# Performance work log

Measured on AMD Instinct MI355X. Metric: run time of the kernel, lower is better.

## Reference

```python
import jax, jax.numpy as jnp
import numpy as np

B, S, D_IN, D_OUT = 4, 2048, 1024, 1024


def setup_inputs() -> dict:
    key = jax.random.key(0)
    ks = jax.random.split(key, 7)
    s_in = 1.0 / np.sqrt(D_IN)
    return {
        "x": jax.random.normal(ks[0], (B, S, D_IN), dtype=jnp.float32),
        "Wq": jax.random.uniform(ks[1], (D_IN, D_OUT), jnp.float32, -s_in, s_in),
        "bq": jax.random.uniform(ks[2], (D_OUT,), jnp.float32, -s_in, s_in),
        "Wk": jax.random.uniform(ks[3], (D_IN, D_OUT), jnp.float32, -s_in, s_in),
        "bk": jax.random.uniform(ks[4], (D_OUT,), jnp.float32, -s_in, s_in),
        "Wv": jax.random.uniform(ks[5], (D_IN, D_OUT), jnp.float32, -s_in, s_in),
        "bv": jax.random.uniform(ks[6], (D_OUT,), jnp.float32, -s_in, s_in),
    }


def reference(x, Wq, bq, Wk, bk, Wv, bv):
    # Linear projections (torch Linear: x @ W^T + b; here W stored as [in,out])
    q = x @ Wq + bq  # [B,S,D]
    k = x @ Wk + bk
    v = x @ Wv + bv
    scores = jnp.einsum("bqd,bkd->bqk", q, k)  # [B,S,S]
    # causal mask: positions j > i masked with -inf (applied BEFORE scaling,
    # which is equivalent since -inf/sqrt(d) == -inf)
    seq = scores.shape[-1]
    causal = jnp.tril(jnp.ones((seq, seq), dtype=bool))
    masked = jnp.where(causal, scores, -jnp.inf)
    attn = jax.nn.softmax(masked / np.sqrt(k.shape[-1]), axis=-1)
    # dropout p=0.0 -> identity
    return attn @ v  # [B,S,D]
```

## Files before the change

kernel.cpp:

```cpp
#include <hip/hip_runtime.h>

typedef unsigned short u16;
typedef unsigned int u32;
typedef __attribute__((ext_vector_type(8))) short short8;
typedef __attribute__((ext_vector_type(4))) float f32x4;

__device__ __forceinline__ u16 f2bf(float f) {
    u32 u = __float_as_uint(f);
    u32 r = (u + 0x7fffu + ((u >> 16) & 1u)) >> 16;
    return (u16)r;
}
__device__ __forceinline__ float bf2f(u16 h) {
    return __uint_as_float(((u32)h) << 16);
}

__device__ __forceinline__ void gld16(u16* lds_dst, const u16* g_src) {
    __builtin_amdgcn_global_load_lds(
        (const __attribute__((address_space(1))) unsigned int*)g_src,
        (__attribute__((address_space(3))) unsigned int*)lds_dst,
        16, 0, 0);
}

__global__ void split_x_k(const float* __restrict__ x, u16* __restrict__ xh,
                          u16* __restrict__ xl) {
    long i = ((long)blockIdx.x * 256 + threadIdx.x) * 4;
    float4 f = *(const float4*)(x + i);
    u16 h0 = f2bf(f.x), h1 = f2bf(f.y), h2 = f2bf(f.z), h3 = f2bf(f.w);
    u16 l0 = f2bf(f.x - bf2f(h0)), l1 = f2bf(f.y - bf2f(h1));
    u16 l2 = f2bf(f.z - bf2f(h2)), l3 = f2bf(f.w - bf2f(h3));
    uint2 hv, lv;
    hv.x = (u32)h0 | ((u32)h1 << 16); hv.y = (u32)h2 | ((u32)h3 << 16);
    lv.x = (u32)l0 | ((u32)l1 << 16); lv.y = (u32)l2 | ((u32)l3 << 16);
    *(uint2*)(xh + i) = hv;
    *(uint2*)(xl + i) = lv;
}

__global__ void splitT_w_k(const float* __restrict__ Wq, const float* __restrict__ Wk,
                           const float* __restrict__ Wv, u16* __restrict__ wth,
                           u16* __restrict__ wtl) {
    __shared__ float tile[32][33];
    int z = blockIdx.z;
    const float* W = (z == 0) ? Wq : (z == 1) ? Wk : Wv;
    int n0 = blockIdx.x * 32, k0 = blockIdx.y * 32;
    int tx = threadIdx.x, ty = threadIdx.y;
#pragma unroll
    for (int r0 = 0; r0 < 4; ++r0) {
        int r = ty + r0 * 8;
        tile[r][tx] = W[(long)(k0 + r) * 1024 + n0 + tx];
    }
    __syncthreads();
    long zoff = (long)z * 1024 * 1024;
#pragma unroll
    for (int r0 = 0; r0 < 4; ++r0) {
        int r = ty + r0 * 8;
        float f = tile[tx][r];
        u16 h = f2bf(f), l = f2bf(f - bf2f(h));
        long idx = zoff + (long)(n0 + r) * 1024 + k0 + tx;
        wth[idx] = h;
        wtl[idx] = l;
    }
}

__global__ void transpose_v_k(const u16* __restrict__ vh, const u16* __restrict__ vl,
                              u16* __restrict__ vth, u16* __restrict__ vtl) {
    __shared__ u16 th[32][33];
    __shared__ u16 tl[32][33];
    int z = blockIdx.z;
    int d0 = blockIdx.x * 32, s0 = blockIdx.y * 32;
    int tx = threadIdx.x, ty = threadIdx.y;
#pragma unroll
    for (int r0 = 0; r0 < 4; ++r0) {
        int r = ty + r0 * 8;
        long idx = ((long)z * 2048 + s0 + r) * 1024 + d0 + tx;
        th[r][tx] = vh[idx];
        tl[r][tx] = vl[idx];
    }
    __syncthreads();
    long zoff = (long)z * 1024 * 2048;
#pragma unroll
    for (int r0 = 0; r0 < 4; ++r0) {
        int r = ty + r0 * 8;
        long idx = zoff + (long)(d0 + r) * 2048 + s0 + tx;
        vth[idx] = th[tx][r];
        vtl[idx] = tl[tx][r];
    }
}

template <int MODE, int NF>
__launch_bounds__(512, 2)
__global__ void gemm_k(const u16* __restrict__ Ah, const u16* __restrict__ Al, long sAz,
                       const u16* __restrict__ Bh, const u16* __restrict__ Bl, long sBz,
                       int lda, int ldb, int Ksize,
                       float* __restrict__ outF, long sCz, int ldc,
                       u16* __restrict__ oh0, u16* __restrict__ oh1, u16* __restrict__ oh2,
                       u16* __restrict__ ol0, u16* __restrict__ ol1, u16* __restrict__ ol2,
                       const float* __restrict__ b0, const float* __restrict__ b1,
                       const float* __restrict__ b2) {
    constexpr int BN = NF * 64;
    constexpr int SLOT = 8192 + NF * 4096;
    constexpr int RING = (MODE == 0) ? 3 : 2;
    __shared__ u16 lds[RING * SLOT];

    const int bi = (MODE == 2) ? (gridDim.x - 1 - (int)blockIdx.x) : blockIdx.x;
    const int bj = blockIdx.y, z = blockIdx.z;
    if (MODE == 1 && bj > bi) return;
    int nsteps = Ksize / 32;
    if (MODE == 2) nsteps = min(nsteps, (bi + 1) * 4);

    const u16* gA_h = Ah + (long)z * sAz;
    const u16* gA_l = Al + (long)z * sAz;
    const u16* gB_h = Bh + (long)z * sBz;
    const u16* gB_l = Bl + (long)z * sBz;

    const int tid = threadIdx.x;
    const int lane = tid & 63, w = tid >> 6;
    const int wr = w >> 2, wc = w & 3;

    const int srow = tid >> 2;
    const int ls8 = (((tid & 3) ^ ((tid >> 3) & 3)) << 3);
    const long aoff  = ((long)bi * 128 + srow) * lda + ls8;
    const long boff0 = ((long)bj * BN + srow) * ldb + ls8;
    const long boff1 = boff0 + 128L * (long)ldb;
    const int wbase = w * 512;

    f32x4 acc[4][NF] = {};

    const int fr = lane & 15;
    const int ps8 = (((lane >> 4) ^ ((fr >> 1) & 3)) << 3);

    auto stage = [&](int slot, int step) {
        const int k0 = step * 32;
        u16* sb = lds + slot * SLOT;
        gld16(sb + wbase,              gA_h + aoff + k0);
        gld16(sb + 4096 + wbase,       gA_l + aoff + k0);
        gld16(sb + 8192 + wbase,       gB_h + boff0 + k0);
        if constexpr (NF == 4) gld16(sb + 12288 + wbase, gB_h + boff1 + k0);
        gld16(sb + 8192 + NF * 2048 + wbase, gB_l + boff0 + k0);
        if constexpr (NF == 4) gld16(sb + 8192 + NF * 2048 + 4096 + wbase, gB_l + boff1 + k0);
    };

    auto compute = [&](int slot) {
        const u16* LA = lds + slot * SLOT;
        const u16* LB = LA + 8192;
        short8 afh[4], afl[4], bfh[NF], bfl[NF];
#pragma unroll
        for (int m = 0; m < 4; ++m) {
            int off = (wr * 64 + m * 16 + fr) * 32 + ps8;
            afh[m] = *(const short8*)(LA + off);
            afl[m] = *(const short8*)(LA + 4096 + off);
        }
#pragma unroll
        for (int n = 0; n < NF; ++n) {
            int off = (wc * (NF * 16) + n * 16 + fr) * 32 + ps8;
            bfh[n] = *(const short8*)(LB + off);
            bfl[n] = *(const short8*)(LB + NF * 2048 + off);
        }
        __builtin_amdgcn_s_setprio(1);
#pragma unroll
        for (int m = 0; m < 4; ++m)
#pragma unroll
            for (int n = 0; n < NF; ++n) {
                acc[m][n] = __builtin_amdgcn_mfma_f32_16x16x32_bf16(afh[m], bfh[n], acc[m][n], 0, 0, 0);
                acc[m][n] = __builtin_amdgcn_mfma_f32_16x16x32_bf16(afh[m], bfl[n], acc[m][n], 0, 0, 0);
                acc[m][n] = __builtin_amdgcn_mfma_f32_16x16x32_bf16(afl[m], bfh[n], acc[m][n], 0, 0, 0);
            }
        __builtin_amdgcn_s_setprio(0);
    };

    if constexpr (MODE == 0) {
        stage(0, 0);
        if (nsteps > 1) stage(1, 1);
        int cs = 0, ns = 2;
        for (int h = 0; h < nsteps; ++h) {
            if (h + 1 < nsteps) {
                asm volatile("s_waitcnt vmcnt(6)" ::: "memory");
            } else {
                asm volatile("s_waitcnt vmcnt(0)" ::: "memory");
            }
            __builtin_amdgcn_s_barrier();
            __builtin_amdgcn_sched_barrier(0);
            if (h + 2 < nsteps) stage(ns, h + 2);
            compute(cs);
            cs = (cs == 2) ? 0 : cs + 1;
            ns = (ns == 2) ? 0 : ns + 1;
        }
    } else {
        stage(0, 0);
        int cs = 0;
        for (int h = 0; h < nsteps; ++h) {
            asm volatile("s_waitcnt vmcnt(0)" ::: "memory");
            __builtin_amdgcn_s_barrier();
            __builtin_amdgcn_sched_barrier(0);
            if (h + 1 < nsteps) stage(cs ^ 1, h + 1);
            compute(cs);
            cs ^= 1;
        }
    }

    const int row0 = bi * 128 + wr * 64 + (lane >> 4) * 4;
    const int col0 = bj * BN + wc * (NF * 16) + (lane & 15);

    if (MODE == 0) {
        const float* bias = (z == 0) ? b0 : (z == 1) ? b1 : b2;
        u16* oh = (z == 0) ? oh0 : (z == 1) ? oh1 : oh2;
        u16* ol = (z == 0) ? ol0 : (z == 1) ? ol1 : ol2;
#pragma unroll
        for (int n = 0; n < NF; ++n) {
            float bv = bias[col0 + n * 16];
#pragma unroll
            for (int m = 0; m < 4; ++m)
#pragma unroll
                for (int j = 0; j < 4; ++j) {
                    float v = acc[m][n][j] + bv;
                    long idx = (long)(row0 + m * 16 + j) * ldc + col0 + n * 16;
                    u16 h = f2bf(v);
                    oh[idx] = h;
                    ol[idx] = f2bf(v - bf2f(h));
                }
        }
    } else {
        float* o = outF + (long)z * sCz;
#pragma unroll
        for (int m = 0; m < 4; ++m)
#pragma unroll
            for (int n = 0; n < NF; ++n)
#pragma unroll
                for (int j = 0; j < 4; ++j)
                    o[(long)(row0 + m * 16 + j) * ldc + col0 + n * 16] = acc[m][n][j];
    }
}

__global__ void softmax_k(const float* __restrict__ S, u16* __restrict__ Ph,
                          u16* __restrict__ Pl) {
    const long row = blockIdx.x;
    const int i = (int)(row & 2047);
    const float* srow = S + row * 2048;
    u16* ph = Ph + row * 2048;
    u16* pl = Pl + row * 2048;
    const int t = threadIdx.x;
    const int limit = ((i >> 7) + 1) << 7;

    float v[8];
    float m = -1e30f;
#pragma unroll
    for (int j = 0; j < 8; ++j) {
        int c = j * 256 + t;
        float x = (c <= i) ? srow[c] : -1e30f;
        v[j] = x;
        m = fmaxf(m, x);
    }
#pragma unroll
    for (int off = 32; off; off >>= 1) m = fmaxf(m, __shfl_xor(m, off));
    __shared__ float redm[4], reds[4];
    if ((t & 63) == 0) redm[t >> 6] = m;
    __syncthreads();
    m = fmaxf(fmaxf(redm[0], redm[1]), fmaxf(redm[2], redm[3]));

    float p[8];
    float s = 0.f;
#pragma unroll
    for (int j = 0; j < 8; ++j) {
        int c = j * 256 + t;
        float e = (c <= i) ? __expf((v[j] - m) * 0.03125f) : 0.f;
        p[j] = e;
        s += e;
    }
#pragma unroll
    for (int off = 32; off; off >>= 1) s += __shfl_xor(s, off);
    if ((t & 63) == 0) reds[t >> 6] = s;
    __syncthreads();
    s = reds[0] + reds[1] + reds[2] + reds[3];
    const float inv = 1.f / s;
#pragma unroll
    for (int j = 0; j < 8; ++j) {
        int c = j * 256 + t;
        if (c < limit) {
            float o = p[j] * inv;
            u16 h = f2bf(o);
            ph[c] = h;
            pl[c] = f2bf(o - bf2f(h));
        }
    }
}

extern "C" void kernel_launch(void* const* d_in, const int* in_sizes, int n_in,
                              void* d_out, int out_size, void* d_ws, size_t ws_size,
                              hipStream_t stream) {
    const float* x  = (const float*)d_in[0];
    const float* Wq = (const float*)d_in[1];
    const float* bq = (const float*)d_in[2];
    const float* Wk = (const float*)d_in[3];
    const float* bk = (const float*)d_in[4];
    const float* Wv = (const float*)d_in[5];
    const float* bv = (const float*)d_in[6];
    float* out = (float*)d_out;
    char* ws = (char*)d_ws;
    const size_t MB = 1ull << 20;

    u16* xs_hi = (u16*)(ws + 0 * MB);
    u16* xs_lo = (u16*)(ws + 16 * MB);
    u16* wt_hi = (u16*)(ws + 32 * MB);
    u16* wt_lo = (u16*)(ws + 38 * MB);
    float* S   = (float*)(ws + 0 * MB);
    u16* q_hi = (u16*)(ws + 64 * MB);
    u16* q_lo = (u16*)(ws + 80 * MB);
    u16* k_hi = (u16*)(ws + 96 * MB);
    u16* k_lo = (u16*)(ws + 112 * MB);
    u16* P_hi = (u16*)(ws + 64 * MB);
    u16* P_lo = (u16*)(ws + 96 * MB);
    u16* v_hi  = (u16*)(ws + 128 * MB);
    u16* v_lo  = (u16*)(ws + 144 * MB);
    u16* vt_hi = (u16*)(ws + 160 * MB);
    u16* vt_lo = (u16*)(ws + 176 * MB);

    split_x_k<<<8192, 256, 0, stream>>>(x, xs_hi, xs_lo);
    splitT_w_k<<<dim3(32, 32, 3), dim3(32, 8), 0, stream>>>(Wq, Wk, Wv, wt_hi, wt_lo);
    gemm_k<0, 4><<<dim3(64, 4, 3), 512, 0, stream>>>(
        xs_hi, xs_lo, 0L, wt_hi, wt_lo, 1024L * 1024, 1024, 1024, 1024,
        nullptr, 0L, 1024, q_hi, k_hi, v_hi, q_lo, k_lo, v_lo, bq, bk, bv);
    transpose_v_k<<<dim3(32, 64, 4), dim3(32, 8), 0, stream>>>(v_hi, v_lo, vt_hi, vt_lo);
    gemm_k<1, 2><<<dim3(16, 16, 4), 512, 0, stream>>>(
        q_hi, q_lo, 2048L * 1024, k_hi, k_lo, 2048L * 1024, 1024, 1024, 1024,
        S, 2048L * 2048, 2048, nullptr, nullptr, nullptr, nullptr, nullptr, nullptr,
        nullptr, nullptr, nullptr);
    softmax_k<<<8192, 256, 0, stream>>>(S, P_hi, P_lo);
    gemm_k<2, 2><<<dim3(16, 8, 4), 512, 0, stream>>>(
        P_hi, P_lo, 2048L * 2048, vt_hi, vt_lo, 1024L * 2048, 2048, 2048, 2048,
        out, 2048L * 1024, 1024, nullptr, nullptr, nullptr, nullptr, nullptr, nullptr,
        nullptr, nullptr, nullptr);
}
```

Measured before the change: 443.9 us.

## Fuse softmax normalization into PV GEMM via row statistics kernel

Splits softmax into a row-reduction kernel that stores only the max and inverse sum per row, and moves the exponentiation and bf16 hi/lo split of P into the PV GEMM, which reads fp32 scores, converts them in registers and writes them straight to LDS. This removes writing and re-reading the two bf16 P matrices. The QK kernel also gains a block-index swizzle for locality. The templated GEMM is specialised into dedicated kernels. In exchange the PV kernel loads fp32 S (twice the bytes of bf16) and recomputes exp per tile. Its loop is serialized on a vmcnt(0) wait plus register writes to LDS, which may reduce overlap.

```diff
diff --git a/kernel.cpp b/kernel.cpp
--- a/kernel.cpp
+++ b/kernel.cpp
@@ -86,31 +86,25 @@
     }
 }
 
-template <int MODE, int NF>
 __launch_bounds__(512, 2)
-__global__ void gemm_k(const u16* __restrict__ Ah, const u16* __restrict__ Al, long sAz,
-                       const u16* __restrict__ Bh, const u16* __restrict__ Bl, long sBz,
-                       int lda, int ldb, int Ksize,
-                       float* __restrict__ outF, long sCz, int ldc,
+__global__ void gemm_k(const u16* __restrict__ Ah, const u16* __restrict__ Al,
+                       const u16* __restrict__ Bh, const u16* __restrict__ Bl,
                        u16* __restrict__ oh0, u16* __restrict__ oh1, u16* __restrict__ oh2,
                        u16* __restrict__ ol0, u16* __restrict__ ol1, u16* __restrict__ ol2,
                        const float* __restrict__ b0, const float* __restrict__ b1,
                        const float* __restrict__ b2) {
-    constexpr int BN = NF * 64;
+    constexpr int NF = 4;
+    constexpr int BN = 256;
     constexpr int SLOT = 8192 + NF * 4096;
-    constexpr int RING = (MODE == 0) ? 3 : 2;
-    __shared__ u16 lds[RING * SLOT];
-
-    const int bi = (MODE == 2) ? (gridDim.x - 1 - (int)blockIdx.x) : blockIdx.x;
-    const int bj = blockIdx.y, z = blockIdx.z;
-    if (MODE == 1 && bj > bi) return;
-    int nsteps = Ksize / 32;
-    if (MODE == 2) nsteps = min(nsteps, (bi + 1) * 4);
-
-    const u16* gA_h = Ah + (long)z * sAz;
-    const u16* gA_l = Al + (long)z * sAz;
-    const u16* gB_h = Bh + (long)z * sBz;
-    const u16* gB_l = Bl + (long)z * sBz;
+    __shared__ u16 lds[3 * SLOT];
+
+    const int bi = blockIdx.x, bj = blockIdx.y, z = blockIdx.z;
+    const int nsteps = 32;
+
+    const u16* gA_h = Ah;
+    const u16* gA_l = Al;
+    const u16* gB_h = Bh + (long)z * 1024 * 1024;
+    const u16* gB_l = Bl + (long)z * 1024 * 1024;
 
     const int tid = threadIdx.x;
     const int lane = tid & 63, w = tid >> 6;
@@ -118,9 +112,9 @@
 
     const int srow = tid >> 2;
     const int ls8 = (((tid & 3) ^ ((tid >> 3) & 3)) << 3);
-    const long aoff  = ((long)bi * 128 + srow) * lda + ls8;
-    const long boff0 = ((long)bj * BN + srow) * ldb + ls8;
-    const long boff1 = boff0 + 128L * (long)ldb;
+    const long aoff  = ((long)bi * 128 + srow) * 1024 + ls8;
+    const long boff0 = ((long)bj * BN + srow) * 1024 + ls8;
+    const long boff1 = boff0 + 128L * 1024;
     const int wbase = w * 512;
 
     f32x4 acc[4][NF] = {};
@@ -131,12 +125,12 @@
     auto stage = [&](int slot, int step) {
         const int k0 = step * 32;
         u16* sb = lds + slot * SLOT;
-        gld16(sb + wbase,              gA_h + aoff + k0);
-        gld16(sb + 4096 + wbase,       gA_l + aoff + k0);
-        gld16(sb + 8192 + wbase,       gB_h + boff0 + k0);
-        if constexpr (NF == 4) gld16(sb + 12288 + wbase, gB_h + boff1 + k0);
-        gld16(sb + 8192 + NF * 2048 + wbase, gB_l + boff0 + k0);
-        if constexpr (NF == 4) gld16(sb + 8192 + NF * 2048 + 4096 + wbase, gB_l + boff1 + k0);
+        gld16(sb + wbase,               gA_h + aoff + k0);
+        gld16(sb + 4096 + wbase,        gA_l + aoff + k0);
+        gld16(sb + 8192 + wbase,        gB_h + boff0 + k0);
+        gld16(sb + 12288 + wbase,       gB_h + boff1 + k0);
+        gld16(sb + 16384 + wbase,       gB_l + boff0 + k0);
+        gld16(sb + 20480 + wbase,       gB_l + boff1 + k0);
     };
 
     auto compute = [&](int slot) {
@@ -167,78 +161,142 @@
         __builtin_amdgcn_s_setprio(0);
     };
 
-    if constexpr (MODE == 0) {
-        stage(0, 0);
-        if (nsteps > 1) stage(1, 1);
-        int cs = 0, ns = 2;
-        for (int h = 0; h < nsteps; ++h) {
-            if (h + 1 < nsteps) {
-                asm volatile("s_waitcnt vmcnt(6)" ::: "memory");
-            } else {
-                asm volatile("s_waitcnt vmcnt(0)" ::: "memory");
-            }
-            __builtin_amdgcn_s_barrier();
-            __builtin_amdgcn_sched_barrier(0);
-            if (h + 2 < nsteps) stage(ns, h + 2);
-            compute(cs);
-            cs = (cs == 2) ? 0 : cs + 1;
-            ns = (ns == 2) ? 0 : ns + 1;
-        }
-    } else {
-        stage(0, 0);
-        int cs = 0;
-        for (int h = 0; h < nsteps; ++h) {
+    stage(0, 0);
+    stage(1, 1);
+    int cs = 0, ns = 2;
+    for (int h = 0; h < nsteps; ++h) {
+        if (h + 1 < nsteps) {
+            asm volatile("s_waitcnt vmcnt(6)" ::: "memory");
+        } else {
             asm volatile("s_waitcnt vmcnt(0)" ::: "memory");
-            __builtin_amdgcn_s_barrier();
-            __builtin_amdgcn_sched_barrier(0);
-            if (h + 1 < nsteps) stage(cs ^ 1, h + 1);
-            compute(cs);
-            cs ^= 1;
-        }
+        }
+        __builtin_amdgcn_s_barrier();
+        __builtin_amdgcn_sched_barrier(0);
+        if (h + 2 < nsteps) stage(ns, h + 2);
+        compute(cs);
+        cs = (cs == 2) ? 0 : cs + 1;
+        ns = (ns == 2) ? 0 : ns + 1;
     }
 
     const int row0 = bi * 128 + wr * 64 + (lane >> 4) * 4;
     const int col0 = bj * BN + wc * (NF * 16) + (lane & 15);
 
-    if (MODE == 0) {
-        const float* bias = (z == 0) ? b0 : (z == 1) ? b1 : b2;
-        u16* oh = (z == 0) ? oh0 : (z == 1) ? oh1 : oh2;
-        u16* ol = (z == 0) ? ol0 : (z == 1) ? ol1 : ol2;
-#pragma unroll
-        for (int n = 0; n < NF; ++n) {
-            float bv = bias[col0 + n * 16];
-#pragma unroll
-            for (int m = 0; m < 4; ++m)
-#pragma unroll
-                for (int j = 0; j < 4; ++j) {
-                    float v = acc[m][n][j] + bv;
-                    long idx = (long)(row0 + m * 16 + j) * ldc + col0 + n * 16;
-                    u16 h = f2bf(v);
-                    oh[idx] = h;
-                    ol[idx] = f2bf(v - bf2f(h));
-                }
-        }
-    } else {
-        float* o = outF + (long)z * sCz;
+    const float* bias = (z == 0) ? b0 : (z == 1) ? b1 : b2;
+    u16* oh = (z == 0) ? oh0 : (z == 1) ? oh1 : oh2;
+    u16* ol = (z == 0) ? ol0 : (z == 1) ? ol1 : ol2;
+#pragma unroll
+    for (int n = 0; n < NF; ++n) {
+        float bv = bias[col0 + n * 16];
 #pragma unroll
         for (int m = 0; m < 4; ++m)
 #pragma unroll
-            for (int n = 0; n < NF; ++n)
-#pragma unroll
-                for (int j = 0; j < 4; ++j)
-                    o[(long)(row0 + m * 16 + j) * ldc + col0 + n * 16] = acc[m][n][j];
-    }
-}
-
-__global__ void softmax_k(const float* __restrict__ S, u16* __restrict__ Ph,
-                          u16* __restrict__ Pl) {
+            for (int j = 0; j < 4; ++j) {
+                float v = acc[m][n][j] + bv;
+                long idx = (long)(row0 + m * 16 + j) * 1024 + col0 + n * 16;
+                u16 h = f2bf(v);
+                oh[idx] = h;
+                ol[idx] = f2bf(v - bf2f(h));
+            }
+    }
+}
+
+__launch_bounds__(512, 2)
+__global__ void qk_k(const u16* __restrict__ Qh, const u16* __restrict__ Ql,
+                     const u16* __restrict__ Kh, const u16* __restrict__ Kl,
+                     float* __restrict__ S) {
+    constexpr int SLOT = 16384;
+    __shared__ u16 lds[2 * SLOT];
+
+    const int orig = blockIdx.y * 16 + blockIdx.x;
+    const int swz = (orig & 7) * 32 + (orig >> 3);
+    const int bi = swz & 15, bj = swz >> 4, z = blockIdx.z;
+    if (bj > bi) return;
+    const int nsteps = 32;
+
+    const u16* gA_h = Qh + (long)z * 2048 * 1024;
+    const u16* gA_l = Ql + (long)z * 2048 * 1024;
+    const u16* gB_h = Kh + (long)z * 2048 * 1024;
+    const u16* gB_l = Kl + (long)z * 2048 * 1024;
+
+    const int tid = threadIdx.x;
+    const int lane = tid & 63, w = tid >> 6;
+    const int wr = w >> 2, wc = w & 3;
+
+    const int srow = tid >> 2;
+    const int ls8 = (((tid & 3) ^ ((tid >> 3) & 3)) << 3);
+    const long aoff  = ((long)bi * 128 + srow) * 1024 + ls8;
+    const long boff0 = ((long)bj * 128 + srow) * 1024 + ls8;
+    const int wbase = w * 512;
+
+    f32x4 acc[4][2] = {};
+    const int fr = lane & 15;
+    const int ps8 = (((lane >> 4) ^ ((fr >> 1) & 3)) << 3);
+
+    auto stage = [&](int slot, int step) {
+        const int k0 = step * 32;
+        u16* sb = lds + slot * SLOT;
+        gld16(sb + wbase,         gA_h + aoff + k0);
+        gld16(sb + 4096 + wbase,  gA_l + aoff + k0);
+        gld16(sb + 8192 + wbase,  gB_h + boff0 + k0);
+        gld16(sb + 12288 + wbase, gB_l + boff0 + k0);
+    };
+
+    auto compute = [&](int slot) {
+        const u16* LA = lds + slot * SLOT;
+        const u16* LB = LA + 8192;
+        short8 afh[4], afl[4], bfh[2], bfl[2];
+#pragma unroll
+        for (int m = 0; m < 4; ++m) {
+            int off = (wr * 64 + m * 16 + fr) * 32 + ps8;
+            afh[m] = *(const short8*)(LA + off);
+            afl[m] = *(const short8*)(LA + 4096 + off);
+        }
+#pragma unroll
+        for (int n = 0; n < 2; ++n) {
+            int off = (wc * 32 + n * 16 + fr) * 32 + ps8;
+            bfh[n] = *(const short8*)(LB + off);
+            bfl[n] = *(const short8*)(LB + 4096 + off);
+        }
+        __builtin_amdgcn_s_setprio(1);
+#pragma unroll
+        for (int m = 0; m < 4; ++m)
+#pragma unroll
+            for (int n = 0; n < 2; ++n) {
+                acc[m][n] = __builtin_amdgcn_mfma_f32_16x16x32_bf16(afh[m], bfh[n], acc[m][n], 0, 0, 0);
+                acc[m][n] = __builtin_amdgcn_mfma_f32_16x16x32_bf16(afh[m], bfl[n], acc[m][n], 0, 0, 0);
+                acc[m][n] = __builtin_amdgcn_mfma_f32_16x16x32_bf16(afl[m], bfh[n], acc[m][n], 0, 0, 0);
+            }
+        __builtin_amdgcn_s_setprio(0);
+    };
+
+    stage(0, 0);
+    int cs = 0;
+    for (int h = 0; h < nsteps; ++h) {
+        asm volatile("s_waitcnt vmcnt(0)" ::: "memory");
+        __builtin_amdgcn_s_barrier();
+        __builtin_amdgcn_sched_barrier(0);
+        if (h + 1 < nsteps) stage(cs ^ 1, h + 1);
+        compute(cs);
+        cs ^= 1;
+    }
+
+    const int row0 = bi * 128 + wr * 64 + (lane >> 4) * 4;
+    const int col0 = bj * 128 + wc * 32 + (lane & 15);
+    float* o = S + (long)z * 2048 * 2048;
+#pragma unroll
+    for (int m = 0; m < 4; ++m)
+#pragma unroll
+        for (int n = 0; n < 2; ++n)
+#pragma unroll
+            for (int j = 0; j < 4; ++j)
+                o[(long)(row0 + m * 16 + j) * 2048 + col0 + n * 16] = acc[m][n][j];
+}
+
+__global__ void rowred_k(const float* __restrict__ S, float2* __restrict__ stats) {
     const long row = blockIdx.x;
     const int i = (int)(row & 2047);
     const float* srow = S + row * 2048;
-    u16* ph = Ph + row * 2048;
-    u16* pl = Pl + row * 2048;
     const int t = threadIdx.x;
-    const int limit = ((i >> 7) + 1) << 7;
 
     float v[8];
     float m = -1e30f;
@@ -256,13 +314,11 @@
     __syncthreads();
     m = fmaxf(fmaxf(redm[0], redm[1]), fmaxf(redm[2], redm[3]));
 
-    float p[8];
     float s = 0.f;
 #pragma unroll
     for (int j = 0; j < 8; ++j) {
         int c = j * 256 + t;
         float e = (c <= i) ? __expf((v[j] - m) * 0.03125f) : 0.f;
-        p[j] = e;
         s += e;
     }
 #pragma unroll
@@ -270,17 +326,130 @@
     if ((t & 63) == 0) reds[t >> 6] = s;
     __syncthreads();
     s = reds[0] + reds[1] + reds[2] + reds[3];
-    const float inv = 1.f / s;
-#pragma unroll
-    for (int j = 0; j < 8; ++j) {
-        int c = j * 256 + t;
-        if (c < limit) {
-            float o = p[j] * inv;
-            u16 h = f2bf(o);
-            ph[c] = h;
-            pl[c] = f2bf(o - bf2f(h));
-        }
-    }
+    if (t == 0) stats[row] = make_float2(m, 1.f / s);
+}
+
+__launch_bounds__(512, 2)
+__global__ void pv_k(const float* __restrict__ S, const float2* __restrict__ stats,
+                     const u16* __restrict__ Vth, const u16* __restrict__ Vtl,
+                     float* __restrict__ out) {
+    constexpr int SLOT = 16384;
+    __shared__ u16 lds[2 * SLOT];
+
+    const int bi = 15 - (int)blockIdx.x;
+    const int bj = blockIdx.y, z = blockIdx.z;
+    const int nsteps = (bi + 1) * 4;
+
+    const float* gS = S + (long)z * 2048 * 2048;
+    const float2* gst = stats + (long)z * 2048;
+    const u16* gB_h = Vth + (long)z * 1024 * 2048;
+    const u16* gB_l = Vtl + (long)z * 1024 * 2048;
+
+    const int tid = threadIdx.x;
+    const int lane = tid & 63, w = tid >> 6;
+    const int wr = w >> 2, wc = w & 3;
+
+    const int srow = tid >> 2;
+    const int ls8 = (((tid & 3) ^ ((tid >> 3) & 3)) << 3);
+    const int arow = bi * 128 + srow;
+    const long arowoff = (long)arow * 2048;
+    const long boff0 = ((long)bj * 128 + srow) * 2048 + ls8;
+    const int wbase = w * 512;
+
+    const float2 st = gst[arow];
+    const float mrow = st.x, inv = st.y;
+
+    f32x4 acc[4][2] = {};
+    const int fr = lane & 15;
+    const int ps8 = (((lane >> 4) ^ ((fr >> 1) & 3)) << 3);
+
+    float4 sv0, sv1;
+
+    auto loadS = [&](int step) {
+        const float* p = gS + arowoff + step * 32 + ls8;
+        sv0 = *(const float4*)p;
+        sv1 = *(const float4*)(p + 4);
+    };
+    auto stageV = [&](int slot, int step) {
+        u16* sb = lds + slot * SLOT;
+        gld16(sb + 8192 + wbase,  gB_h + boff0 + step * 32);
+        gld16(sb + 12288 + wbase, gB_l + boff0 + step * 32);
+    };
+    auto writeP = [&](int slot, int step) {
+        const int c0 = step * 32 + ls8;
+        float sf[8] = {sv0.x, sv0.y, sv0.z, sv0.w, sv1.x, sv1.y, sv1.z, sv1.w};
+        u16 h8[8], l8[8];
+#pragma unroll
+        for (int e = 0; e < 8; ++e) {
+            float p = ((c0 + e) <= arow) ? __expf((sf[e] - mrow) * 0.03125f) * inv : 0.f;
+            u16 h = f2bf(p);
+            h8[e] = h;
+            l8[e] = f2bf(p - bf2f(h));
+        }
+        u16* sb = lds + slot * SLOT;
+        *(short8*)(sb + wbase + lane * 8)        = *(const short8*)h8;
+        *(short8*)(sb + 4096 + wbase + lane * 8) = *(const short8*)l8;
+    };
+    auto compute = [&](int slot) {
+        const u16* LA = lds + slot * SLOT;
+        const u16* LB = LA + 8192;
+        short8 afh[4], afl[4], bfh[2], bfl[2];
+#pragma unroll
+        for (int m = 0; m < 4; ++m) {
+            int off = (wr * 64 + m * 16 + fr) * 32 + ps8;
+            afh[m] = *(const short8*)(LA + off);
+            afl[m] = *(const short8*)(LA + 4096 + off);
+        }
+#pragma unroll
+        for (int n = 0; n < 2; ++n) {
+            int off = (wc * 32 + n * 16 + fr) * 32 + ps8;
+            bfh[n] = *(const short8*)(LB + off);
+            bfl[n] = *(const short8*)(LB + 4096 + off);
+        }
+        __builtin_amdgcn_s_setprio(1);
+#pragma unroll
+        for (int m = 0; m < 4; ++m)
+#pragma unroll
+            for (int n = 0; n < 2; ++n) {
+                acc[m][n] = __builtin_amdgcn_mfma_f32_16x16x32_bf16(afh[m], bfh[n], acc[m][n], 0, 0, 0);
+                acc[m][n] = __builtin_amdgcn_mfma_f32_16x16x32_bf16(afh[m], bfl[n], acc[m][n], 0, 0, 0);
+                acc[m][n] = __builtin_amdgcn_mfma_f32_16x16x32_bf16(afl[m], bfh[n], acc[m][n], 0, 0, 0);
+            }
+        __builtin_amdgcn_s_setprio(0);
+    };
+
+    loadS(0);
+    stageV(0, 0);
+    asm volatile("s_waitcnt vmcnt(0)" ::: "memory");
+    writeP(0, 0);
+    asm volatile("s_waitcnt lgkmcnt(0)" ::: "memory");
+    __builtin_amdgcn_s_barrier();
+    __builtin_amdgcn_sched_barrier(0);
+
+    int cs = 0;
+    for (int h = 0; h < nsteps; ++h) {
+        if (h + 1 < nsteps) { loadS(h + 1); stageV(cs ^ 1, h + 1); }
+        compute(cs);
+        if (h + 1 < nsteps) {
+            asm volatile("s_waitcnt vmcnt(0)" ::: "memory");
+            writeP(cs ^ 1, h + 1);
+            asm volatile("s_waitcnt lgkmcnt(0)" ::: "memory");
+        }
+        __builtin_amdgcn_s_barrier();
+        __builtin_amdgcn_sched_barrier(0);
+        cs ^= 1;
+    }
+
+    const int row0 = bi * 128 + wr * 64 + (lane >> 4) * 4;
+    const int col0 = bj * 128 + wc * 32 + (lane & 15);
+    float* o = out + (long)z * 2048 * 1024;
+#pragma unroll
+    for (int m = 0; m < 4; ++m)
+#pragma unroll
+        for (int n = 0; n < 2; ++n)
+#pragma unroll
+            for (int j = 0; j < 4; ++j)
+                o[(long)(row0 + m * 16 + j) * 1024 + col0 + n * 16] = acc[m][n][j];
 }
 
 extern "C" void kernel_launch(void* const* d_in, const int* in_sizes, int n_in,
@@ -306,8 +475,7 @@
     u16* q_lo = (u16*)(ws + 80 * MB);
     u16* k_hi = (u16*)(ws + 96 * MB);
     u16* k_lo = (u16*)(ws + 112 * MB);
-    u16* P_hi = (u16*)(ws + 64 * MB);
-    u16* P_lo = (u16*)(ws + 96 * MB);
+    float2* stats = (float2*)(ws + 64 * MB);
     u16* v_hi  = (u16*)(ws + 128 * MB);
     u16* v_lo  = (u16*)(ws + 144 * MB);
     u16* vt_hi = (u16*)(ws + 160 * MB);
@@ -315,17 +483,10 @@
 
     split_x_k<<<8192, 256, 0, stream>>>(x, xs_hi, xs_lo);
     splitT_w_k<<<dim3(32, 32, 3), dim3(32, 8), 0, stream>>>(Wq, Wk, Wv, wt_hi, wt_lo);
-    gemm_k<0, 4><<<dim3(64, 4, 3), 512, 0, stream>>>(
-        xs_hi, xs_lo, 0L, wt_hi, wt_lo, 1024L * 1024, 1024, 1024, 1024,
-        nullptr, 0L, 1024, q_hi, k_hi, v_hi, q_lo, k_lo, v_lo, bq, bk, bv);
+    gemm_k<<<dim3(64, 4, 3), 512, 0, stream>>>(
+        xs_hi, xs_lo, wt_hi, wt_lo, q_hi, k_hi, v_hi, q_lo, k_lo, v_lo, bq, bk, bv);
     transpose_v_k<<<dim3(32, 64, 4), dim3(32, 8), 0, stream>>>(v_hi, v_lo, vt_hi, vt_lo);
-    gemm_k<1, 2><<<dim3(16, 16, 4), 512, 0, stream>>>(
-        q_hi, q_lo, 2048L * 1024, k_hi, k_lo, 2048L * 1024, 1024, 1024, 1024,
-        S, 2048L * 2048, 2048, nullptr, nullptr, nullptr, nullptr, nullptr, nullptr,
-        nullptr, nullptr, nullptr);
-    softmax_k<<<8192, 256, 0, stream>>>(S, P_hi, P_lo);
-    gemm_k<2, 2><<<dim3(16, 8, 4), 512, 0, stream>>>(
-        P_hi, P_lo, 2048L * 2048, vt_hi, vt_lo, 1024L * 2048, 2048, 2048, 2048,
-        out, 2048L * 1024, 1024, nullptr, nullptr, nullptr, nullptr, nullptr, nullptr,
-        nullptr, nullptr, nullptr);
-}
+    qk_k<<<dim3(16, 16, 4), 512, 0, stream>>>(q_hi, q_lo, k_hi, k_lo, S);
+    rowred_k<<<8192, 256, 0, stream>>>(S, stats);
+    pv_k<<<dim3(16, 8, 4), 512, 0, stream>>>(S, stats, vt_hi, vt_lo, out);
+}
```

New measurement: 488.6 us. +10.1%, slower.
